# Performance work log

Measured on AMD Instinct MI355X. Metric: run time of the kernel, lower is better.

## Reference

```python
import jax, jax.numpy as jnp
import numpy as np

N = 8192       # nodes per graph
E = 262144     # edges per graph (avg degree 32)
H = 8          # attention heads
C = 128        # hidden dim per head (H*C = 1024 to match Linear(1024,128))
IN = 128       # input feature dim
NEG_SLOPE = 0.2


def _gat_conv(x, edge_index, W, att_src, att_dst, bias):
    """PyG GATConv (concat=True, add_self_loops=True, shared lin for src/dst)."""
    n = x.shape[0]
    loop = jnp.arange(n, dtype=edge_index.dtype)
    src = jnp.concatenate([edge_index[0], loop])  # [E+N]
    dst = jnp.concatenate([edge_index[1], loop])
    h = (x @ W).reshape(n, H, C)                         # [N,H,C]
    a_src = jnp.sum(h * att_src, axis=-1)                # [N,H]
    a_dst = jnp.sum(h * att_dst, axis=-1)                # [N,H]
    e = jax.nn.leaky_relu(a_src[src] + a_dst[dst], NEG_SLOPE)   # [E+N,H]
    m = jax.ops.segment_max(e, dst, num_segments=n)      # per-dst max for stability
    ex = jnp.exp(e - m[dst])
    den = jax.ops.segment_sum(ex, dst, num_segments=n)
    alpha = ex / den[dst]                                # [E+N,H] neighborhood softmax
    out = jax.ops.segment_sum(h[src] * alpha[:, :, None], dst, num_segments=n)
    return out.reshape(n, H * C) + bias                  # [N, H*C]


def setup_inputs() -> dict:
    key = jax.random.key(0)
    ks = jax.random.split(key, 12)
    s = 0.05  # keep activations in a sane range
    return {
        "x1": jax.random.normal(ks[0], (N, IN), jnp.float32),
        "edge_index1": jax.random.randint(ks[1], (2, E), 0, N, dtype=jnp.int64),
        "W1": jax.random.normal(ks[2], (IN, H * C), jnp.float32) * s,
        "att_src1": jax.random.normal(ks[3], (H, C), jnp.float32) * s,
        "att_dst1": jax.random.normal(ks[4], (H, C), jnp.float32) * s,
        "b1": jnp.zeros((H * C,), jnp.float32),
        "x2": jax.random.normal(ks[5], (N, IN), jnp.float32),
        "edge_index2": jax.random.randint(ks[6], (2, E), 0, N, dtype=jnp.int64),
        "W2": jax.random.normal(ks[7], (IN, H * C), jnp.float32) * s,
        "att_src2": jax.random.normal(ks[8], (H, C), jnp.float32) * s,
        "att_dst2": jax.random.normal(ks[9], (H, C), jnp.float32) * s,
        "b2": jnp.zeros((H * C,), jnp.float32),
        "Wl": jax.random.normal(ks[10], (H * C, 128), jnp.float32) * s,
        "bl": jnp.zeros((128,), jnp.float32),
    }


def reference(x1, edge_index1, W1, att_src1, att_dst1, b1,
              x2, edge_index2, W2, att_src2, att_dst2, b2, Wl, bl):
    emb1 = _gat_conv(x1, edge_index1, W1, att_src1, att_dst1, b1)  # [N1,1024]
    emb2 = _gat_conv(x2, edge_index2, W2, att_src2, att_dst2, b2)  # [N2,1024]
    scores = emb1 @ emb2.T                                          # [N1,N2]
    w1 = jax.nn.softmax(scores, axis=1)
    w2 = jax.nn.softmax(scores, axis=0)
    cross1 = (w2 @ emb2) @ Wl + bl      # [N1,128]
    cross2 = (w1.T @ emb1) @ Wl + bl    # [N2,128]
    return (jnp.mean(cross1, axis=0), jnp.mean(cross2, axis=0))
```

## Files before the change

### kernel.cpp

```cpp
#include <hip/hip_runtime.h>


#define NN 8192
#define EE 262144
#define NEG 0.2f

#define BKT 128
#define RNG (NN / BKT)
#define CAP 2560
#define CHK (EE / 128)

#define U_CNT   0
#define U_GACC  (U_CNT + 4*BKT)
#define U_ZEND  (U_GACC + 2048)
#define U_U     (U_ZEND)
#define U_MEMB  (U_U + 2*2048)
#define U_ASRC  (U_MEMB + 2048)
#define U_ADST  (U_ASRC + 2*NN*8)
#define U_PR    (U_ADST + 2*NN*8)
#define U_BIND  (U_PR + 2*NN*16)
#define U_BINS  (U_BIND + 2*BKT*CAP)
#define ZERO_BYTES ((size_t)U_ZEND * 4)

__global__ __launch_bounds__(1024) void k_bin(
    const int* __restrict__ ei1, const int* __restrict__ ei2,
    const float* __restrict__ W1, const float* __restrict__ as1,
    const float* __restrict__ ad1,
    const float* __restrict__ W2, const float* __restrict__ as2,
    const float* __restrict__ ad2,
    int* __restrict__ cnt, int* __restrict__ binD, int* __restrict__ binS,
    float* __restrict__ u) {
  int g = blockIdx.y;
  int t = threadIdx.x;
  if (blockIdx.x >= 128) {
    int sd = blockIdx.x - 128;
    const float* Wg = g ? W2 : W1;
    const float* att = g ? (sd ? ad2 : as2) : (sd ? ad1 : as1);
    float* uo = u + g * 2048 + sd * 1024;
    int head = t >> 7, k = t & 127;
    const float4* wr = (const float4*)(Wg + (size_t)k * 1024 + head * 128);
    const float4* ar = (const float4*)(att + head * 128);
    float s = 0.f;
#pragma unroll 8
    for (int c = 0; c < 32; ++c) {
      float4 w4 = wr[c], a4 = ar[c];
      s += w4.x * a4.x + w4.y * a4.y + w4.z * a4.z + w4.w * a4.w;
    }
    uo[t] = s;
    return;
  }
  const int* ei = g ? ei2 : ei1;
  __shared__ int hD[BKT], hS[BKT], bD[BKT], bS[BKT];
  if (t < BKT) { hD[t] = 0; hS[t] = 0; }
  __syncthreads();
  int e0 = blockIdx.x * CHK;
  int sE[2], dE[2], lD[2], lS[2];
#pragma unroll
  for (int uu = 0; uu < 2; ++uu) {
    int i = e0 + uu * 1024 + t;
    sE[uu] = ei[i];
    dE[uu] = ei[EE + i];
  }
#pragma unroll
  for (int uu = 0; uu < 2; ++uu) {
    lD[uu] = atomicAdd(&hD[dE[uu] >> 6], 1);
    lS[uu] = atomicAdd(&hS[sE[uu] >> 6], 1);
  }
  __syncthreads();
  if (t < BKT) {
    bD[t] = atomicAdd(cnt + (2 * g + 0) * BKT + t, hD[t]);
    bS[t] = atomicAdd(cnt + (2 * g + 1) * BKT + t, hS[t]);
  }
  __syncthreads();
  int* bdg = binD + (size_t)g * BKT * CAP;
  int* bsg = binS + (size_t)g * BKT * CAP;
#pragma unroll
  for (int uu = 0; uu < 2; ++uu) {
    int kb = dE[uu] >> 6;
    bdg[kb * CAP + bD[kb] + lD[uu]] = (sE[uu] << 6) | (dE[uu] & 63);
    kb = sE[uu] >> 6;
    bsg[kb * CAP + bS[kb] + lS[uu]] = (dE[uu] << 6) | (sE[uu] & 63);
  }
}

__global__ __launch_bounds__(1024) void k_a(
    const float* __restrict__ x1, const float* __restrict__ x2,
    const float* __restrict__ u,
    float* __restrict__ asrc, float* __restrict__ adst) {
  int gph = blockIdx.y, cb = blockIdx.x;
  __shared__ float xs[64][129];
  __shared__ float us[16][128];
  int t = threadIdx.x;
  const float* ug = u + gph * 2048;
  for (int i = t; i < 2048; i += 1024) us[i >> 7][i & 127] = ug[i];
  const float* x = gph ? x2 : x1;
  const int n0 = cb * 64;
  const float4* xb4 = (const float4*)(x + (size_t)n0 * 128);
  for (int i = t; i < 64 * 32; i += 1024) {
    float4 v = xb4[i];
    int r = i >> 5, c = (i & 31) * 4;
    xs[r][c] = v.x; xs[r][c + 1] = v.y; xs[r][c + 2] = v.z; xs[r][c + 3] = v.w;
  }
  __syncthreads();
  int nl = t & 63;
  int j0 = t >> 6;
  float a0 = 0.f;
#pragma unroll 4
  for (int k = 0; k < 128; ++k) a0 += xs[nl][k] * us[j0][k];
  int n = n0 + nl;
  if (j0 < 8) asrc[gph * (NN * 8) + n * 8 + j0] = a0;
  else        adst[gph * (NN * 8) + n * 8 + (j0 - 8)] = a0;
}

__global__ __launch_bounds__(1024) void k_den(
    const int* __restrict__ cnt, const int* __restrict__ binD,
    const float* __restrict__ asrc, const float* __restrict__ adst,
    float* __restrict__ pr) {
  int gph = blockIdx.y, b = blockIdx.x;
  int lo = b * RNG;
  const float* as = asrc + gph * (NN * 8);
  const float* ad = adst + gph * (NN * 8);
  float2* prg = (float2*)pr + (size_t)gph * (NN * 8);
  __shared__ float den[RNG * 8];
  __shared__ float ads[RNG * 8];
  int t = threadIdx.x;
  if (t < RNG * 8) {
    float avv = ad[lo * 8 + t];
    float v = as[lo * 8 + t] + avv;
    v = v > 0.f ? v : NEG * v;
    ads[t] = avv;
    den[t] = __expf(v);
  }
  __syncthreads();
  int n = cnt[(2 * gph + 0) * BKT + b];
  const int* recs = binD + (size_t)gph * BKT * CAP + b * CAP;
  int rid = t >> 3, h = t & 7;
  for (int base = 0; base < n; base += 512) {
    int rv[4]; bool ok[4]; float sv[4];
#pragma unroll
    for (int uu = 0; uu < 4; ++uu) {
      int i = base + uu * 128 + rid;
      ok[uu] = i < n;
      rv[uu] = ok[uu] ? recs[i] : 0;
    }
#pragma unroll
    for (int uu = 0; uu < 4; ++uu)
      sv[uu] = ok[uu] ? as[(rv[uu] >> 6) * 8 + h] : 0.f;
#pragma unroll
    for (int uu = 0; uu < 4; ++uu) {
      if (ok[uu]) {
        int dl = rv[uu] & 63;
        float v = sv[uu] + ads[dl * 8 + h];
        v = v > 0.f ? v : NEG * v;
        atomicAdd(&den[dl * 8 + h], __expf(v));
      }
    }
  }
  __syncthreads();
  if (t < RNG * 8)
    prg[lo * 8 + t] = make_float2(ads[t], 1.0f / den[t]);
}

__global__ __launch_bounds__(1024) void k_waccG(
    const int* __restrict__ cnt, const int* __restrict__ binS,
    const float* __restrict__ asrc, const float* __restrict__ pr,
    const float* __restrict__ x1, const float* __restrict__ x2,
    float* __restrict__ gacc) {
  int gph = blockIdx.y, b = blockIdx.x;
  int lo = b * RNG;
  const float* as = asrc + gph * (NN * 8);
  const float2* prg = (const float2*)pr + (size_t)gph * (NN * 8);
  __shared__ float wv[RNG * 8];
  __shared__ float asx[RNG * 8];
  int t = threadIdx.x;
  if (t < RNG * 8) {
    float sva = as[lo * 8 + t];
    float2 f2 = prg[lo * 8 + t];
    float v = sva + f2.x;
    v = v > 0.f ? v : NEG * v;
    asx[t] = sva;
    wv[t] = __expf(v) * f2.y;
  }
  __syncthreads();
  int n = cnt[(2 * gph + 1) * BKT + b];
  const int* recs = binS + (size_t)gph * BKT * CAP + b * CAP;
  int rid = t >> 3, h = t & 7;
  for (int base = 0; base < n; base += 512) {
    int rv[4]; bool ok[4]; float2 pv[4];
#pragma unroll
    for (int uu = 0; uu < 4; ++uu) {
      int i = base + uu * 128 + rid;
      ok[uu] = i < n;
      rv[uu] = ok[uu] ? recs[i] : 0;
    }
#pragma unroll
    for (int uu = 0; uu < 4; ++uu)
      pv[uu] = ok[uu] ? prg[(size_t)(rv[uu] >> 6) * 8 + h] : make_float2(0.f, 0.f);
#pragma unroll
    for (int uu = 0; uu < 4; ++uu) {
      if (ok[uu]) {
        int sl = rv[uu] & 63;
        float v = asx[sl * 8 + h] + pv[uu].x;
        v = v > 0.f ? v : NEG * v;
        atomicAdd(&wv[sl * 8 + h], __expf(v) * pv[uu].y);
      }
    }
  }
  __syncthreads();
  const float* x = gph ? x2 : x1;
  float* gg = gacc + gph * 1024;
  int k = t & 127;
  int h0 = t >> 7;
  int n0 = b * RNG;
  float a0 = 0.f;
#pragma unroll 4
  for (int nl = 0; nl < RNG; ++nl)
    a0 += x[(size_t)(n0 + nl) * 128 + k] * wv[nl * 8 + h0];
  atomicAdd(gg + h0 * 128 + k, a0);
}

__global__ __launch_bounds__(512) void k_memb(
    const float* __restrict__ gacc,
    const float* __restrict__ W1, const float* __restrict__ b1,
    const float* __restrict__ W2, const float* __restrict__ b2,
    float* __restrict__ memb) {
  int g = blockIdx.y;
  int e0 = blockIdx.x * 64;
  const float* W = g ? W2 : W1;
  const float* bb = g ? b2 : b1;
  const float* gr = gacc + g * 1024 + (e0 >> 7) * 128;
  __shared__ float pm[8][64];
  int t = threadIdx.x;
  int el = t & 63, kc = t >> 6;
  int e = e0 + el;
  float s = 0.f;
#pragma unroll
  for (int k = kc * 16; k < kc * 16 + 16; ++k)
    s += gr[k] * W[(size_t)k * 1024 + e];
  pm[kc][el] = s;
  __syncthreads();
  if (t < 64) {
    float acc = pm[0][el];
#pragma unroll
    for (int q = 1; q < 8; ++q) acc += pm[q][el];
    memb[g * 1024 + e] = acc * (1.0f / (float)NN) + bb[e];
  }
}

__global__ __launch_bounds__(512) void k_out(
    const float* __restrict__ memb, const float* __restrict__ Wl,
    const float* __restrict__ bl, float* __restrict__ out) {
  __shared__ float ml[1024];
  __shared__ float po[16][32];
  int b = blockIdx.x;
  int t = threadIdx.x;
  const float* m = (b < 4) ? (memb + 1024) : memb;
  for (int i = t; i < 1024; i += 512) ml[i] = m[i];
  __syncthreads();
  int ol = t & 31, kc = t >> 5;
  int o = b * 32 + ol;
  int j = o & 127;
  float s = 0.f;
#pragma unroll 8
  for (int k = kc * 64; k < kc * 64 + 64; ++k)
    s += ml[k] * Wl[(size_t)k * 128 + j];
  po[kc][ol] = s;
  __syncthreads();
  if (t < 32) {
    float acc = po[0][t];
#pragma unroll
    for (int q = 1; q < 16; ++q) acc += po[q][t];
    out[b * 32 + t] = acc + bl[(b * 32 + t) & 127];
  }
}

extern "C" void kernel_launch(void* const* d_in, const int* in_sizes, int n_in,
                              void* d_out, int out_size, void* d_ws, size_t ws_size,
                              hipStream_t stream) {
  const float* x1  = (const float*)d_in[0];
  const int*   ei1 = (const int*)d_in[1];
  const float* W1  = (const float*)d_in[2];
  const float* as1 = (const float*)d_in[3];
  const float* ad1 = (const float*)d_in[4];
  const float* b1  = (const float*)d_in[5];
  const float* x2  = (const float*)d_in[6];
  const int*   ei2 = (const int*)d_in[7];
  const float* W2  = (const float*)d_in[8];
  const float* as2 = (const float*)d_in[9];
  const float* ad2 = (const float*)d_in[10];
  const float* b2  = (const float*)d_in[11];
  const float* Wl  = (const float*)d_in[12];
  const float* bl  = (const float*)d_in[13];
  float* out = (float*)d_out;

  int*   cnt  = (int*)d_ws + U_CNT;
  float* gacc = (float*)d_ws + U_GACC;
  float* u    = (float*)d_ws + U_U;
  float* memb = (float*)d_ws + U_MEMB;
  float* asrc = (float*)d_ws + U_ASRC;
  float* adst = (float*)d_ws + U_ADST;
  float* pr   = (float*)d_ws + U_PR;
  int*   binD = (int*)d_ws + U_BIND;
  int*   binS = (int*)d_ws + U_BINS;

  hipMemsetAsync(d_ws, 0, ZERO_BYTES, stream);

  k_bin<<<dim3(130, 2), 1024, 0, stream>>>(ei1, ei2, W1, as1, ad1,
                                           W2, as2, ad2, cnt, binD, binS, u);
  k_a<<<dim3(128, 2), 1024, 0, stream>>>(x1, x2, u, asrc, adst);
  k_den<<<dim3(BKT, 2), 1024, 0, stream>>>(cnt, binD, asrc, adst, pr);
  k_waccG<<<dim3(BKT, 2), 1024, 0, stream>>>(cnt, binS, asrc, pr, x1, x2, gacc);
  k_memb<<<dim3(16, 2), 512, 0, stream>>>(gacc, W1, b1, W2, b2, memb);
  k_out<<<8, 512, 0, stream>>>(memb, Wl, bl, out);
}
```

Baseline: 181.3 us.

## Replace memset with zeroing kernel and fuse binning with attention-logit projection

Measured after the change: 178.1 us. About the same (-1.8%).

```diff
diff --git a/kernel.cpp b/kernel.cpp
--- a/kernel.cpp
+++ b/kernel.cpp
@@ -12,32 +12,34 @@
 
 #define U_CNT   0
 #define U_GACC  (U_CNT + 4*BKT)
-#define U_ZEND  (U_GACC + 2048)
-#define U_U     (U_ZEND)
+#define U_U     (U_GACC + 2048)
 #define U_MEMB  (U_U + 2*2048)
 #define U_ASRC  (U_MEMB + 2048)
 #define U_ADST  (U_ASRC + 2*NN*8)
 #define U_PR    (U_ADST + 2*NN*8)
 #define U_BIND  (U_PR + 2*NN*16)
 #define U_BINS  (U_BIND + 2*BKT*CAP)
-#define ZERO_BYTES ((size_t)U_ZEND * 4)
-
-__global__ __launch_bounds__(1024) void k_bin(
-    const int* __restrict__ ei1, const int* __restrict__ ei2,
+
+__global__ __launch_bounds__(512) void k_pre(
     const float* __restrict__ W1, const float* __restrict__ as1,
     const float* __restrict__ ad1,
     const float* __restrict__ W2, const float* __restrict__ as2,
     const float* __restrict__ ad2,
-    int* __restrict__ cnt, int* __restrict__ binD, int* __restrict__ binS,
-    float* __restrict__ u) {
-  int g = blockIdx.y;
-  int t = threadIdx.x;
-  if (blockIdx.x >= 128) {
-    int sd = blockIdx.x - 128;
-    const float* Wg = g ? W2 : W1;
-    const float* att = g ? (sd ? ad2 : as2) : (sd ? ad1 : as1);
-    float* uo = u + g * 2048 + sd * 1024;
-    int head = t >> 7, k = t & 127;
+    int* __restrict__ cnt, float* __restrict__ gacc, float* __restrict__ u) {
+  int t = threadIdx.x;
+  if (blockIdx.x == 0) {
+    cnt[t] = 0;
+#pragma unroll
+    for (int i = t; i < 2048; i += 512) gacc[i] = 0.f;
+    return;
+  }
+  int id = blockIdx.x - 1;
+  int g = id >> 1, sd = id & 1;
+  const float* Wg = g ? W2 : W1;
+  const float* att = g ? (sd ? ad2 : as2) : (sd ? ad1 : as1);
+  float* uo = u + g * 2048 + sd * 1024;
+  for (int o = t; o < 1024; o += 512) {
+    int head = o >> 7, k = o & 127;
     const float4* wr = (const float4*)(Wg + (size_t)k * 1024 + head * 128);
     const float4* ar = (const float4*)(att + head * 128);
     float s = 0.f;
@@ -46,70 +48,86 @@
       float4 w4 = wr[c], a4 = ar[c];
       s += w4.x * a4.x + w4.y * a4.y + w4.z * a4.z + w4.w * a4.w;
     }
-    uo[t] = s;
+    uo[o] = s;
+  }
+}
+
+union SMemBA {
+  struct { int hD[BKT]; int hS[BKT]; int bD[BKT]; int bS[BKT]; } bin;
+  struct { float xs[64][129]; float us[16][128]; } a;
+};
+
+__global__ __launch_bounds__(512) void k_binA(
+    const int* __restrict__ ei1, const int* __restrict__ ei2,
+    const float* __restrict__ x1, const float* __restrict__ x2,
+    const float* __restrict__ u,
+    int* __restrict__ cnt, int* __restrict__ binD, int* __restrict__ binS,
+    float* __restrict__ asrc, float* __restrict__ adst) {
+  __shared__ SMemBA sm;
+  int g = blockIdx.y;
+  int t = threadIdx.x;
+
+  if (blockIdx.x >= 128) {
+    int cb = blockIdx.x - 128;
+    const float* ug = u + g * 2048;
+    for (int i = t; i < 2048; i += 512) sm.a.us[i >> 7][i & 127] = ug[i];
+    const float* x = g ? x2 : x1;
+    const int n0 = cb * 64;
+    const float4* xb4 = (const float4*)(x + (size_t)n0 * 128);
+    for (int i = t; i < 64 * 32; i += 512) {
+      float4 v = xb4[i];
+      int r = i >> 5, c = (i & 31) * 4;
+      sm.a.xs[r][c] = v.x; sm.a.xs[r][c + 1] = v.y;
+      sm.a.xs[r][c + 2] = v.z; sm.a.xs[r][c + 3] = v.w;
+    }
+    __syncthreads();
+    int nl = t & 63;
+    int j0 = (t >> 6) * 2;
+    float a0 = 0.f, a1 = 0.f;
+#pragma unroll 4
+    for (int k = 0; k < 128; ++k) {
+      float xv = sm.a.xs[nl][k];
+      a0 += xv * sm.a.us[j0 + 0][k];
+      a1 += xv * sm.a.us[j0 + 1][k];
+    }
+    int n = n0 + nl;
+    float* outp = (j0 < 8) ? (asrc + g * (NN * 8) + n * 8 + j0)
+                           : (adst + g * (NN * 8) + n * 8 + (j0 - 8));
+    outp[0] = a0; outp[1] = a1;
     return;
   }
+
   const int* ei = g ? ei2 : ei1;
-  __shared__ int hD[BKT], hS[BKT], bD[BKT], bS[BKT];
-  if (t < BKT) { hD[t] = 0; hS[t] = 0; }
+  for (int i = t; i < BKT; i += 512) { sm.bin.hD[i] = 0; sm.bin.hS[i] = 0; }
   __syncthreads();
   int e0 = blockIdx.x * CHK;
-  int sE[2], dE[2], lD[2], lS[2];
-#pragma unroll
-  for (int uu = 0; uu < 2; ++uu) {
-    int i = e0 + uu * 1024 + t;
+  int sE[4], dE[4], lD[4], lS[4];
+#pragma unroll
+  for (int uu = 0; uu < 4; ++uu) {
+    int i = e0 + uu * 512 + t;
     sE[uu] = ei[i];
     dE[uu] = ei[EE + i];
   }
 #pragma unroll
-  for (int uu = 0; uu < 2; ++uu) {
-    lD[uu] = atomicAdd(&hD[dE[uu] >> 6], 1);
-    lS[uu] = atomicAdd(&hS[sE[uu] >> 6], 1);
-  }
-  __syncthreads();
-  if (t < BKT) {
-    bD[t] = atomicAdd(cnt + (2 * g + 0) * BKT + t, hD[t]);
-    bS[t] = atomicAdd(cnt + (2 * g + 1) * BKT + t, hS[t]);
+  for (int uu = 0; uu < 4; ++uu) {
+    lD[uu] = atomicAdd(&sm.bin.hD[dE[uu] >> 6], 1);
+    lS[uu] = atomicAdd(&sm.bin.hS[sE[uu] >> 6], 1);
+  }
+  __syncthreads();
+  for (int i = t; i < BKT; i += 512) {
+    sm.bin.bD[i] = atomicAdd(cnt + (2 * g + 0) * BKT + i, sm.bin.hD[i]);
+    sm.bin.bS[i] = atomicAdd(cnt + (2 * g + 1) * BKT + i, sm.bin.hS[i]);
   }
   __syncthreads();
   int* bdg = binD + (size_t)g * BKT * CAP;
   int* bsg = binS + (size_t)g * BKT * CAP;
 #pragma unroll
-  for (int uu = 0; uu < 2; ++uu) {
+  for (int uu = 0; uu < 4; ++uu) {
     int kb = dE[uu] >> 6;
-    bdg[kb * CAP + bD[kb] + lD[uu]] = (sE[uu] << 6) | (dE[uu] & 63);
+    bdg[kb * CAP + sm.bin.bD[kb] + lD[uu]] = (sE[uu] << 6) | (dE[uu] & 63);
     kb = sE[uu] >> 6;
-    bsg[kb * CAP + bS[kb] + lS[uu]] = (dE[uu] << 6) | (sE[uu] & 63);
-  }
-}
-
-__global__ __launch_bounds__(1024) void k_a(
-    const float* __restrict__ x1, const float* __restrict__ x2,
-    const float* __restrict__ u,
-    float* __restrict__ asrc, float* __restrict__ adst) {
-  int gph = blockIdx.y, cb = blockIdx.x;
-  __shared__ float xs[64][129];
-  __shared__ float us[16][128];
-  int t = threadIdx.x;
-  const float* ug = u + gph * 2048;
-  for (int i = t; i < 2048; i += 1024) us[i >> 7][i & 127] = ug[i];
-  const float* x = gph ? x2 : x1;
-  const int n0 = cb * 64;
-  const float4* xb4 = (const float4*)(x + (size_t)n0 * 128);
-  for (int i = t; i < 64 * 32; i += 1024) {
-    float4 v = xb4[i];
-    int r = i >> 5, c = (i & 31) * 4;
-    xs[r][c] = v.x; xs[r][c + 1] = v.y; xs[r][c + 2] = v.z; xs[r][c + 3] = v.w;
-  }
-  __syncthreads();
-  int nl = t & 63;
-  int j0 = t >> 6;
-  float a0 = 0.f;
-#pragma unroll 4
-  for (int k = 0; k < 128; ++k) a0 += xs[nl][k] * us[j0][k];
-  int n = n0 + nl;
-  if (j0 < 8) asrc[gph * (NN * 8) + n * 8 + j0] = a0;
-  else        adst[gph * (NN * 8) + n * 8 + (j0 - 8)] = a0;
+    bsg[kb * CAP + sm.bin.bS[kb] + lS[uu]] = (dE[uu] << 6) | (sE[uu] & 63);
+  }
 }
 
 __global__ __launch_bounds__(1024) void k_den(
@@ -303,11 +321,9 @@
   int*   binD = (int*)d_ws + U_BIND;
   int*   binS = (int*)d_ws + U_BINS;
 
-  hipMemsetAsync(d_ws, 0, ZERO_BYTES, stream);
-
-  k_bin<<<dim3(130, 2), 1024, 0, stream>>>(ei1, ei2, W1, as1, ad1,
-                                           W2, as2, ad2, cnt, binD, binS, u);
-  k_a<<<dim3(128, 2), 1024, 0, stream>>>(x1, x2, u, asrc, adst);
+  k_pre<<<5, 512, 0, stream>>>(W1, as1, ad1, W2, as2, ad2, cnt, gacc, u);
+  k_binA<<<dim3(256, 2), 512, 0, stream>>>(ei1, ei2, x1, x2, u,
+                                           cnt, binD, binS, asrc, adst);
   k_den<<<dim3(BKT, 2), 1024, 0, stream>>>(cnt, binD, asrc, adst, pr);
   k_waccG<<<dim3(BKT, 2), 1024, 0, stream>>>(cnt, binS, asrc, pr, x1, x2, gacc);
   k_memb<<<dim3(16, 2), 512, 0, stream>>>(gacc, W1, b1, W2, b2, memb);
```
